# Kernel tuning notes

Hardware: AMD Instinct MI355X
Metric: run time of the kernel (lower is better)

## Reference

```python
import jax, jax.numpy as jnp
import numpy as np

N = 20000        # nodes
E = 640000       # edges (before self-loops)
F_IN = 128
HID = 64
HEADS = 4
F_OUT = 128
G = 64           # graphs in batch
NEG_SLOPE = 0.2  # PyG GATConv leaky_relu default


def setup_inputs() -> dict:
    key = jax.random.key(0)
    ks = jax.random.split(key, 16)
    s = 0.05
    x = jax.random.normal(ks[0], (N, F_IN), jnp.float32)
    edge_index = jax.random.randint(ks[1], (2, E), 0, N, dtype=jnp.int64)
    batch = jnp.sort(jax.random.randint(ks[2], (N,), 0, G, dtype=jnp.int64))
    # layer 1: F_IN -> HID x HEADS (concat)
    W1 = jax.random.normal(ks[3], (F_IN, HEADS * HID), jnp.float32) * s
    a_src1 = jax.random.normal(ks[4], (HEADS, HID), jnp.float32) * s
    a_dst1 = jax.random.normal(ks[5], (HEADS, HID), jnp.float32) * s
    b1 = jnp.zeros((HEADS * HID,), jnp.float32)
    # layer 2: HEADS*HID -> HID x HEADS (concat)
    W2 = jax.random.normal(ks[6], (HEADS * HID, HEADS * HID), jnp.float32) * s
    a_src2 = jax.random.normal(ks[7], (HEADS, HID), jnp.float32) * s
    a_dst2 = jax.random.normal(ks[8], (HEADS, HID), jnp.float32) * s
    b2 = jnp.zeros((HEADS * HID,), jnp.float32)
    # layer 3: HEADS*HID -> F_OUT, heads=1, concat=False (mean)
    W3 = jax.random.normal(ks[9], (HEADS * HID, F_OUT), jnp.float32) * s
    a_src3 = jax.random.normal(ks[10], (1, F_OUT), jnp.float32) * s
    a_dst3 = jax.random.normal(ks[11], (1, F_OUT), jnp.float32) * s
    b3 = jnp.zeros((F_OUT,), jnp.float32)
    return dict(x=x, edge_index=edge_index, batch=batch,
                W1=W1, a_src1=a_src1, a_dst1=a_dst1, b1=b1,
                W2=W2, a_src2=a_src2, a_dst2=a_dst2, b2=b2,
                W3=W3, a_src3=a_src3, a_dst3=a_dst3, b3=b3)


def _gat_layer(x, src, dst, W, a_s, a_d, b, heads, concat):
    n = x.shape[0]
    h = (x @ W).reshape(n, heads, -1)                # [N,H,C]
    alpha_s = (h * a_s[None]).sum(-1)                # [N,H]
    alpha_d = (h * a_d[None]).sum(-1)                # [N,H]
    e = jax.nn.leaky_relu(alpha_s[src] + alpha_d[dst], NEG_SLOPE)  # [E,H]
    # segment softmax over incoming edges of each dst node
    m = jax.ops.segment_max(e, dst, num_segments=n)
    ex = jnp.exp(e - m[dst])
    denom = jax.ops.segment_sum(ex, dst, num_segments=n)
    alpha = ex / (denom[dst] + 1e-16)                # [E,H]
    out = jax.ops.segment_sum(alpha[:, :, None] * h[src], dst, num_segments=n)  # [N,H,C]
    out = out.reshape(n, -1) if concat else out.mean(axis=1)
    return out + b


def reference(x, edge_index, batch, W1, a_src1, a_dst1, b1,
              W2, a_src2, a_dst2, b2, W3, a_src3, a_dst3, b3):
    n = x.shape[0]
    # add self loops (PyG GATConv default add_self_loops=True)
    loop = jnp.arange(n, dtype=edge_index.dtype)
    src = jnp.concatenate([edge_index[0], loop])
    dst = jnp.concatenate([edge_index[1], loop])

    h = _gat_layer(x, src, dst, W1, a_src1, a_dst1, b1, HEADS, True)
    h = jax.nn.elu(h)
    h = _gat_layer(h, src, dst, W2, a_src2, a_dst2, b2, HEADS, True)
    h = jax.nn.elu(h)
    h = _gat_layer(h, src, dst, W3, a_src3, a_dst3, b3, 1, False)

    # global mean pool over graphs
    sums = jax.ops.segment_sum(h, batch, num_segments=G)
    cnts = jax.ops.segment_sum(jnp.ones((n, 1), h.dtype), batch, num_segments=G)
    graph_embedding = sums / jnp.maximum(cnts, 1.0)
    return graph_embedding, h
```

## Files before the change

### kernel.cpp

```cpp
#include <hip/hip_runtime.h>
#include <hip/hip_bf16.h>
#include <math.h>

#define N_NODES 20000
#define N_EDGES 640000
#define ET_EDGES (N_EDGES + N_NODES)
#define G_GRAPHS 64
#define NEG_SLOPE 0.2f

typedef __attribute__((ext_vector_type(8))) short s8v;
typedef __attribute__((ext_vector_type(4))) float f4v;

__device__ __forceinline__ unsigned short bf_hi(float f) {
    union { float f; unsigned int u; } c; c.f = f;
    unsigned int r = (c.u + 0x7fffu + ((c.u >> 16) & 1u)) >> 16;
    return (unsigned short)r;
}
__device__ __forceinline__ float bf_f(unsigned short h) {
    union { unsigned int u; float f; } c; c.u = ((unsigned int)h) << 16;
    return c.f;
}


__global__ void hist_dst(const int* __restrict__ ei, int* __restrict__ cnt,
                         const int* __restrict__ batch, int* __restrict__ gstart) {
    int j = blockIdx.x * blockDim.x + threadIdx.x;
    if (blockIdx.x == 0 && threadIdx.x <= G_GRAPHS) {
        int g = threadIdx.x;
        int lo = 0, hi = N_NODES;
        while (lo < hi) {
            int mid = (lo + hi) >> 1;
            if (batch[mid] < g) lo = mid + 1; else hi = mid;
        }
        gstart[g] = lo;
    }
    if (j >= ET_EDGES) return;
    int d = (j < N_EDGES) ? ei[N_EDGES + j] : (j - N_EDGES);
    atomicAdd(&cnt[d], 1);
}

__global__ __launch_bounds__(1024) void scan_rowptr(const int* __restrict__ cnt,
                                                    int* __restrict__ row_ptr) {
    __shared__ int lds[N_NODES];
    __shared__ int sums[1024];
    const int n = N_NODES;
    const int CH = (n + 1023) / 1024;
    int t = threadIdx.x;
    for (int i = t; i < n; i += 1024) lds[i] = cnt[i];
    __syncthreads();
    int base = t * CH;
    int s = 0;
    for (int i = 0; i < CH; ++i) {
        int idx = base + i;
        if (idx < n) s += lds[idx];
    }
    sums[t] = s;
    __syncthreads();
    for (int o = 1; o < 1024; o <<= 1) {
        int v = (t >= o) ? sums[t - o] : 0;
        __syncthreads();
        sums[t] += v;
        __syncthreads();
    }
    int run = (t == 0) ? 0 : sums[t - 1];
    for (int i = 0; i < CH; ++i) {
        int idx = base + i;
        if (idx < n) { int c = lds[idx]; lds[idx] = run; run += c; }
    }
    __syncthreads();
    for (int i = t; i < n; i += 1024) row_ptr[i] = lds[i];
    if (t == 1023) row_ptr[n] = sums[1023];
}

__global__ void fill_csr(const int* __restrict__ ei, const int* __restrict__ row_ptr,
                         int* __restrict__ cur, int* __restrict__ col) {
    int j = blockIdx.x * blockDim.x + threadIdx.x;
    if (j >= ET_EDGES) return;
    int s, d;
    if (j < N_EDGES) { s = ei[j]; d = ei[N_EDGES + j]; }
    else             { s = d = j - N_EDGES; }
    int pos = row_ptr[d] + atomicAdd(&cur[d], 1);
    col[pos] = s;
}


__global__ void prep_split(const float* __restrict__ x,
                           const float* __restrict__ W1, const float* __restrict__ W2,
                           const float* __restrict__ W3,
                           unsigned short* __restrict__ xh, unsigned short* __restrict__ xl,
                           unsigned short* __restrict__ w1h, unsigned short* __restrict__ w1l,
                           unsigned short* __restrict__ w2h, unsigned short* __restrict__ w2l,
                           unsigned short* __restrict__ w3h, unsigned short* __restrict__ w3l,
                           int* __restrict__ cntcur, float* __restrict__ gout,
                           float* __restrict__ a3z) {
    int idx = blockIdx.x * blockDim.x + threadIdx.x;
    if (idx < 640000) {
        int i = idx * 4;
        float4 v = *(const float4*)&x[i];
        ushort4 h, l;
        h.x = bf_hi(v.x); l.x = bf_hi(v.x - bf_f(h.x));
        h.y = bf_hi(v.y); l.y = bf_hi(v.y - bf_f(h.y));
        h.z = bf_hi(v.z); l.z = bf_hi(v.z - bf_f(h.z));
        h.w = bf_hi(v.w); l.w = bf_hi(v.w - bf_f(h.w));
        *(ushort4*)&xh[i] = h;
        *(ushort4*)&xl[i] = l;
        return;
    }
    idx -= 640000;
    if (idx < 32768) {
        int k = idx / 256, n = idx % 256;
        float v = W1[idx];
        unsigned short h = bf_hi(v);
        w1h[n * 128 + k] = h;
        w1l[n * 128 + k] = bf_hi(v - bf_f(h));
        return;
    }
    idx -= 32768;
    if (idx < 65536) {
        int k = idx / 256, n = idx % 256;
        float v = W2[idx];
        unsigned short h = bf_hi(v);
        w2h[n * 256 + k] = h;
        w2l[n * 256 + k] = bf_hi(v - bf_f(h));
        return;
    }
    idx -= 65536;
    if (idx < 32768) {
        int k = idx / 128, n = idx % 128;
        float v = W3[idx];
        unsigned short h = bf_hi(v);
        w3h[n * 256 + k] = h;
        w3l[n * 256 + k] = bf_hi(v - bf_f(h));
        return;
    }
    idx -= 32768;
    if (idx < 10000) {
        *(int4*)&cntcur[idx * 4] = make_int4(0, 0, 0, 0);
        return;
    }
    idx -= 10000;
    if (idx < 2048) {
        *(float4*)&gout[idx * 4] = make_float4(0.f, 0.f, 0.f, 0.f);
        return;
    }
    idx -= 2048;
    if (idx < 10000) {
        *(float4*)&a3z[idx * 4] = make_float4(0.f, 0.f, 0.f, 0.f);
    }
}


#define LDT 40

template <int CPH>
__global__ __launch_bounds__(256) void gemm_split(
        const unsigned short* __restrict__ Ah, const unsigned short* __restrict__ Al,
        const unsigned short* __restrict__ Bh, const unsigned short* __restrict__ Bl,
        float* __restrict__ C, int M, int Nc, int K,
        const float* __restrict__ a_src, const float* __restrict__ a_dst,
        float* __restrict__ asT, float* __restrict__ adT) {
    __shared__ unsigned short lAh[128 * LDT];
    __shared__ unsigned short lAl[128 * LDT];
    __shared__ unsigned short lBh[128 * LDT];
    __shared__ unsigned short lBl[128 * LDT];
    int bm = blockIdx.x * 128, bn = blockIdx.y * 128;
    int t = threadIdx.x, w = t >> 6, lane = t & 63;
    int wm = (w >> 1) * 64, wn = (w & 1) * 64;

    f4v acc[4][4] = {};

    int sr = t >> 1, sk = (t & 1) << 4;
    int ar = bm + sr; if (ar >= M) ar = M - 1;
    const unsigned short* pAh = Ah + (size_t)ar * K + sk;
    const unsigned short* pAl = Al + (size_t)ar * K + sk;
    const unsigned short* pBh = Bh + (size_t)(bn + sr) * K + sk;
    const unsigned short* pBl = Bl + (size_t)(bn + sr) * K + sk;

    int fr = lane & 15, fk = (lane >> 4) << 3;

    uint4 vh0 = *(const uint4*)(pAh + 0);
    uint4 vh1 = *(const uint4*)(pAh + 8);
    uint4 vl0 = *(const uint4*)(pAl + 0);
    uint4 vl1 = *(const uint4*)(pAl + 8);
    uint4 wh0 = *(const uint4*)(pBh + 0);
    uint4 wh1 = *(const uint4*)(pBh + 8);
    uint4 wl0 = *(const uint4*)(pBl + 0);
    uint4 wl1 = *(const uint4*)(pBl + 8);

    for (int k0 = 0; k0 < K; k0 += 32) {
        __syncthreads();
        *(uint4*)&lAh[sr * LDT + sk]     = vh0;
        *(uint4*)&lAh[sr * LDT + sk + 8] = vh1;
        *(uint4*)&lAl[sr * LDT + sk]     = vl0;
        *(uint4*)&lAl[sr * LDT + sk + 8] = vl1;
        *(uint4*)&lBh[sr * LDT + sk]     = wh0;
        *(uint4*)&lBh[sr * LDT + sk + 8] = wh1;
        *(uint4*)&lBl[sr * LDT + sk]     = wl0;
        *(uint4*)&lBl[sr * LDT + sk + 8] = wl1;
        __syncthreads();

        int kn = k0 + 32;
        if (kn < K) {
            vh0 = *(const uint4*)(pAh + kn);
            vh1 = *(const uint4*)(pAh + kn + 8);
            vl0 = *(const uint4*)(pAl + kn);
            vl1 = *(const uint4*)(pAl + kn + 8);
            wh0 = *(const uint4*)(pBh + kn);
            wh1 = *(const uint4*)(pBh + kn + 8);
            wl0 = *(const uint4*)(pBl + kn);
            wl1 = *(const uint4*)(pBl + kn + 8);
        }

        s8v a_h[4], a_l[4], b_h[4], b_l[4];
        #pragma unroll
        for (int mi = 0; mi < 4; ++mi) {
            a_h[mi] = *(const s8v*)&lAh[(wm + mi * 16 + fr) * LDT + fk];
            a_l[mi] = *(const s8v*)&lAl[(wm + mi * 16 + fr) * LDT + fk];
        }
        #pragma unroll
        for (int nj = 0; nj < 4; ++nj) {
            b_h[nj] = *(const s8v*)&lBh[(wn + nj * 16 + fr) * LDT + fk];
            b_l[nj] = *(const s8v*)&lBl[(wn + nj * 16 + fr) * LDT + fk];
        }
        #pragma unroll
        for (int mi = 0; mi < 4; ++mi)
            #pragma unroll
            for (int nj = 0; nj < 4; ++nj) {
                acc[mi][nj] = __builtin_amdgcn_mfma_f32_16x16x32_bf16(
                    a_h[mi], b_h[nj], acc[mi][nj], 0, 0, 0);
                acc[mi][nj] = __builtin_amdgcn_mfma_f32_16x16x32_bf16(
                    a_h[mi], b_l[nj], acc[mi][nj], 0, 0, 0);
                acc[mi][nj] = __builtin_amdgcn_mfma_f32_16x16x32_bf16(
                    a_l[mi], b_h[nj], acc[mi][nj], 0, 0, 0);
            }
    }

    #pragma unroll
    for (int mi = 0; mi < 4; ++mi)
        #pragma unroll
        for (int nj = 0; nj < 4; ++nj) {
            int row0 = bm + wm + mi * 16 + (lane >> 4) * 4;
            int colc = bn + wn + nj * 16 + (lane & 15);
            #pragma unroll
            for (int q = 0; q < 4; ++q) {
                int r = row0 + q;
                if (r < M) C[(size_t)r * Nc + colc] = acc[mi][nj][q];
            }
        }

    float av_s[4], av_d[4];
    #pragma unroll
    for (int nj = 0; nj < 4; ++nj) {
        int aidx = bn + wn + nj * 16 + fr;
        av_s[nj] = a_src[aidx];
        av_d[nj] = a_dst[aidx];
    }
    int head = (bn + wn) / CPH;
    #pragma unroll
    for (int mi = 0; mi < 4; ++mi) {
        #pragma unroll
        for (int q = 0; q < 4; ++q) {
            float ps = acc[mi][0][q] * av_s[0] + acc[mi][1][q] * av_s[1]
                     + acc[mi][2][q] * av_s[2] + acc[mi][3][q] * av_s[3];
            float pd = acc[mi][0][q] * av_d[0] + acc[mi][1][q] * av_d[1]
                     + acc[mi][2][q] * av_d[2] + acc[mi][3][q] * av_d[3];
            #pragma unroll
            for (int o = 1; o < 16; o <<= 1) {
                ps += __shfl_xor(ps, o);
                pd += __shfl_xor(pd, o);
            }
            if (fr == 0) {
                int r = bm + wm + mi * 16 + (lane >> 4) * 4 + q;
                if (r < M) {
                    if (CPH == 64) {
                        asT[(size_t)head * M + r] = ps;
                        adT[(size_t)head * M + r] = pd;
                    } else {
                        atomicAdd(&asT[r], ps);
                        atomicAdd(&adT[r], pd);
                    }
                }
            }
        }
    }
}


template <int NSLICE, int SCH, int F, int HEADS, bool DO_ELU, bool SPLIT>
__global__ __launch_bounds__(256) void gat_aggregate_sliced(
        const float* __restrict__ h,
        const float* __restrict__ asT,
        const float* __restrict__ adT,
        const int* __restrict__ row_ptr,
        const int* __restrict__ col,
        const float* __restrict__ bias,
        float* __restrict__ out,
        unsigned short* __restrict__ oh,
        unsigned short* __restrict__ ol) {
    constexpr int CL = SCH / 4;
    constexpr int E  = 64 / CL;
    constexpr int CPH = F / HEADS;
    __shared__ int   s_off[4][64];
    __shared__ float s_p[4][64];
    int slice = blockIdx.x & (NSLICE - 1);
    int ng = blockIdx.x >> 2;
    int wid = threadIdx.x >> 6, lane = threadIdx.x & 63;
    int v = ng * 4 + wid;
    if (v >= N_NODES) return;
    int head = (slice * SCH) / CPH;
    int eg = lane / CL, cl = lane % CL;
    int r0 = row_ptr[v], r1 = row_ptr[v + 1];
    float ad = adT[head * N_NODES + v];
    const float* asrc = asT + head * N_NODES;
    float acc[4] = {};
    float lsum = 0.f;
    const char* hb = (const char*)(h + slice * SCH + cl * 4);

#define GATHER4(gg)                                                        \
    {                                                                      \
        int k0 = ((gg) + 0) * E + eg;                                      \
        int k1 = ((gg) + 1) * E + eg;                                      \
        int k2 = ((gg) + 2) * E + eg;                                      \
        int k3 = ((gg) + 3) * E + eg;                                      \
        float p0 = s_p[wid][k0]; int o0 = s_off[wid][k0];                  \
        float p1 = s_p[wid][k1]; int o1 = s_off[wid][k1];                  \
        float p2 = s_p[wid][k2]; int o2 = s_off[wid][k2];                  \
        float p3 = s_p[wid][k3]; int o3 = s_off[wid][k3];                  \
        float4 h0 = *(const float4*)(hb + o0);                             \
        float4 h1 = *(const float4*)(hb + o1);                             \
        float4 h2 = *(const float4*)(hb + o2);                             \
        float4 h3 = *(const float4*)(hb + o3);                             \
        acc[0] = fmaf(p0, h0.x, acc[0]);                                   \
        acc[1] = fmaf(p0, h0.y, acc[1]);                                   \
        acc[2] = fmaf(p0, h0.z, acc[2]);                                   \
        acc[3] = fmaf(p0, h0.w, acc[3]);                                   \
        acc[0] = fmaf(p1, h1.x, acc[0]);                                   \
        acc[1] = fmaf(p1, h1.y, acc[1]);                                   \
        acc[2] = fmaf(p1, h1.z, acc[2]);                                   \
        acc[3] = fmaf(p1, h1.w, acc[3]);                                   \
        acc[0] = fmaf(p2, h2.x, acc[0]);                                   \
        acc[1] = fmaf(p2, h2.y, acc[1]);                                   \
        acc[2] = fmaf(p2, h2.z, acc[2]);                                   \
        acc[3] = fmaf(p2, h2.w, acc[3]);                                   \
        acc[0] = fmaf(p3, h3.x, acc[0]);                                   \
        acc[1] = fmaf(p3, h3.y, acc[1]);                                   \
        acc[2] = fmaf(p3, h3.z, acc[2]);                                   \
        acc[3] = fmaf(p3, h3.w, acc[3]);                                   \
    }

    for (int base = r0; base < r1; base += 64) {
        int j = base + lane;
        bool valid = j < r1;
        int s = col[valid ? j : r0];
        float e = asrc[s] + ad;
        e = (e > 0.f) ? e : NEG_SLOPE * e;
        float p = valid ? __expf(e) : 0.f;
        lsum += p;
        s_p[wid][lane] = p;
        s_off[wid][lane] = s * (F * 4);

        int nk = min(64, r1 - base);
        int nkg = (nk + E - 1) / E;
        int g = 0;
        for (; g + 4 <= nkg; g += 4) GATHER4(g);
        if (g < nkg) GATHER4(g);
    }
#undef GATHER4

    #pragma unroll
    for (int o = 32; o; o >>= 1) lsum += __shfl_xor(lsum, o);
    #pragma unroll
    for (int c = 0; c < 4; ++c) {
        #pragma unroll
        for (int o = CL; o < 64; o <<= 1) acc[c] += __shfl_xor(acc[c], o);
    }
    if (eg == 0) {
        float inv = 1.f / (lsum + 1e-16f);
        int ch0 = slice * SCH + cl * 4;
        float o4[4];
        #pragma unroll
        for (int c = 0; c < 4; ++c) {
            float o = acc[c] * inv + bias[ch0 + c];
            if (DO_ELU) o = (o > 0.f) ? o : expm1f(o);
            o4[c] = o;
        }
        if constexpr (SPLIT) {
            ushort4 hv4, lv4;
            hv4.x = bf_hi(o4[0]); lv4.x = bf_hi(o4[0] - bf_f(hv4.x));
            hv4.y = bf_hi(o4[1]); lv4.y = bf_hi(o4[1] - bf_f(hv4.y));
            hv4.z = bf_hi(o4[2]); lv4.z = bf_hi(o4[2] - bf_f(hv4.z));
            hv4.w = bf_hi(o4[3]); lv4.w = bf_hi(o4[3] - bf_f(hv4.w));
            *(ushort4*)&oh[(size_t)v * F + ch0] = hv4;
            *(ushort4*)&ol[(size_t)v * F + ch0] = lv4;
        } else {
            *(float4*)&out[(size_t)v * F + ch0] =
                make_float4(o4[0], o4[1], o4[2], o4[3]);
        }
    }
}


__global__ void pool_mean4(const float* __restrict__ hout, const int* __restrict__ gstart,
                           float* __restrict__ gout) {
    int g = blockIdx.x;
    int q = blockIdx.y;
    int c = threadIdx.x;
    int off = gstart[g], end = gstart[g + 1];
    float inv = 1.f / fmaxf((float)(end - off), 1.0f);
    float s = 0.f;
    for (int i = off + q; i < end; i += 4) s += hout[(size_t)i * 128 + c];
    atomicAdd(&gout[g * 128 + c], s * inv);
}


static inline size_t align_up(size_t x, size_t a) { return (x + a - 1) & ~(a - 1); }

extern "C" void kernel_launch(void* const* d_in, const int* in_sizes, int n_in,
                              void* d_out, int out_size, void* d_ws, size_t ws_size,
                              hipStream_t stream) {
    const float* x   = (const float*)d_in[0];
    const int*   ei  = (const int*)d_in[1];
    const int*   bat = (const int*)d_in[2];
    const float* W1  = (const float*)d_in[3];
    const float* as1 = (const float*)d_in[4];
    const float* ad1 = (const float*)d_in[5];
    const float* b1  = (const float*)d_in[6];
    const float* W2  = (const float*)d_in[7];
    const float* as2 = (const float*)d_in[8];
    const float* ad2 = (const float*)d_in[9];
    const float* b2  = (const float*)d_in[10];
    const float* W3  = (const float*)d_in[11];
    const float* as3 = (const float*)d_in[12];
    const float* ad3 = (const float*)d_in[13];
    const float* b3  = (const float*)d_in[14];

    float* gout = (float*)d_out;
    float* hout = (float*)d_out + G_GRAPHS * 128;

    char* w = (char*)d_ws;
    size_t o = 0;
    float* bufA = (float*)(w + o);           o = align_up(o + (size_t)N_NODES * 256 * 4, 256);
    unsigned short* Bh = (unsigned short*)(w + o); o = align_up(o + (size_t)N_NODES * 256 * 2, 256);
    unsigned short* Bl = (unsigned short*)(w + o); o = align_up(o + (size_t)N_NODES * 256 * 2, 256);
    unsigned short* xh = (unsigned short*)(w + o); o = align_up(o + (size_t)N_NODES * 128 * 2, 256);
    unsigned short* xl = (unsigned short*)(w + o); o = align_up(o + (size_t)N_NODES * 128 * 2, 256);
    unsigned short* Wt1h = (unsigned short*)(w + o); o = align_up(o + (size_t)256 * 128 * 2, 256);
    unsigned short* Wt1l = (unsigned short*)(w + o); o = align_up(o + (size_t)256 * 128 * 2, 256);
    unsigned short* Wt2h = (unsigned short*)(w + o); o = align_up(o + (size_t)256 * 256 * 2, 256);
    unsigned short* Wt2l = (unsigned short*)(w + o); o = align_up(o + (size_t)256 * 256 * 2, 256);
    unsigned short* Wt3h = (unsigned short*)(w + o); o = align_up(o + (size_t)128 * 256 * 2, 256);
    unsigned short* Wt3l = (unsigned short*)(w + o); o = align_up(o + (size_t)128 * 256 * 2, 256);
    float* alpha = (float*)(w + o);
    float* asv1 = alpha;
    float* adv1 = alpha + 4 * N_NODES;
    float* asv2 = alpha + 8 * N_NODES;
    float* adv2 = alpha + 12 * N_NODES;
    float* asv3 = alpha + 16 * N_NODES;
    float* adv3 = alpha + 17 * N_NODES;
    o = align_up(o + (size_t)18 * N_NODES * 4, 256);
    int* row_ptr = (int*)(w + o);  o = align_up(o + (size_t)(N_NODES + 1) * 4, 256);
    int* col     = (int*)(w + o);  o = align_up(o + (size_t)ET_EDGES * 4, 256);
    int* cnt     = (int*)(w + o);  o += (size_t)N_NODES * 4;
    int* cur     = (int*)(w + o);  o = align_up(o + (size_t)N_NODES * 4, 256);
    int* gstart  = (int*)(w + o);  o = align_up(o + (size_t)(G_GRAPHS + 1) * 4, 256);

    {
        int total = 640000 + 32768 + 65536 + 32768 + 10000 + 2048 + 10000;
        prep_split<<<(total + 255) / 256, 256, 0, stream>>>(
            x, W1, W2, W3, xh, xl, Wt1h, Wt1l, Wt2h, Wt2l, Wt3h, Wt3l, cnt, gout, asv3);
    }
    hist_dst<<<(ET_EDGES + 255) / 256, 256, 0, stream>>>(ei, cnt, bat, gstart);
    scan_rowptr<<<1, 1024, 0, stream>>>(cnt, row_ptr);
    fill_csr<<<(ET_EDGES + 255) / 256, 256, 0, stream>>>(ei, row_ptr, cur, col);

    int gm = (N_NODES + 127) / 128;
    int nb = (N_NODES + 3) / 4;
    int nbs = nb * 4;

    gemm_split<64><<<dim3(gm, 2), 256, 0, stream>>>(
        xh, xl, Wt1h, Wt1l, bufA, N_NODES, 256, 128, as1, ad1, asv1, adv1);
    gat_aggregate_sliced<4, 64, 256, 4, true, true><<<nbs, 256, 0, stream>>>(
        bufA, asv1, adv1, row_ptr, col, b1, nullptr, Bh, Bl);

    gemm_split<64><<<dim3(gm, 2), 256, 0, stream>>>(
        Bh, Bl, Wt2h, Wt2l, bufA, N_NODES, 256, 256, as2, ad2, asv2, adv2);
    gat_aggregate_sliced<4, 64, 256, 4, true, true><<<nbs, 256, 0, stream>>>(
        bufA, asv2, adv2, row_ptr, col, b2, nullptr, Bh, Bl);

    gemm_split<128><<<dim3(gm, 1), 256, 0, stream>>>(
        Bh, Bl, Wt3h, Wt3l, bufA, N_NODES, 128, 256, as3, ad3, asv3, adv3);
    gat_aggregate_sliced<4, 32, 128, 1, false, false><<<nbs, 256, 0, stream>>>(
        bufA, asv3, adv3, row_ptr, col, b3, hout, nullptr, nullptr);

    pool_mean4<<<dim3(G_GRAPHS, 4), 128, 0, stream>>>(hout, gstart, gout);
}
```

Before: 399.1 us.

## Fuse CSR build and prep into one cooperative kernel with grid syncs

Replaces the four preprocessing launches (prep_split, hist_dst, scan_rowptr, fill_csr) with a single cooperative kernel of 1024 blocks that separates the phases with grid-wide syncs. The single-block scan over 20000 counts becomes a two-level scan: per-block partial sums, one block scanning the block totals, then each block writing its own row_ptr chunk. This is meant to cut launch gaps and the serial scan cost. In exchange it relies on cooperative launch co-residency for all 1024 blocks, adds five grid.sync barriers, and has one thread per block write its row_ptr chunk serially.

```diff
diff --git a/kernel.cpp b/kernel.cpp
--- a/kernel.cpp
+++ b/kernel.cpp
@@ -1,6 +1,9 @@
 #include <hip/hip_runtime.h>
 #include <hip/hip_bf16.h>
+#include <hip/hip_cooperative_groups.h>
 #include <math.h>
+
+namespace cg = cooperative_groups;
 
 #define N_NODES 20000
 #define N_EDGES 640000
@@ -8,6 +11,9 @@
 #define G_GRAPHS 64
 #define NEG_SLOPE 0.2f
 
+#define NBC 1024
+#define CHC ((N_NODES + NBC - 1) / NBC)
+
 typedef __attribute__((ext_vector_type(8))) short s8v;
 typedef __attribute__((ext_vector_type(4))) float f4v;
 
@@ -22,11 +28,89 @@
 }
 
 
-__global__ void hist_dst(const int* __restrict__ ei, int* __restrict__ cnt,
-                         const int* __restrict__ batch, int* __restrict__ gstart) {
-    int j = blockIdx.x * blockDim.x + threadIdx.x;
-    if (blockIdx.x == 0 && threadIdx.x <= G_GRAPHS) {
-        int g = threadIdx.x;
+__global__ void __launch_bounds__(256) build_all(
+        const float* __restrict__ x,
+        const float* __restrict__ W1, const float* __restrict__ W2,
+        const float* __restrict__ W3,
+        const int* __restrict__ ei, const int* __restrict__ batch,
+        unsigned short* __restrict__ xh, unsigned short* __restrict__ xl,
+        unsigned short* __restrict__ w1h, unsigned short* __restrict__ w1l,
+        unsigned short* __restrict__ w2h, unsigned short* __restrict__ w2l,
+        unsigned short* __restrict__ w3h, unsigned short* __restrict__ w3l,
+        int* __restrict__ cntcur,
+        float* __restrict__ gout, float* __restrict__ a3z,
+        int* __restrict__ row_ptr, int* __restrict__ col,
+        int* __restrict__ gstart, int* __restrict__ bsum) {
+    cg::grid_group grid = cg::this_grid();
+    __shared__ int l2[NBC];
+    __shared__ int ps[256];
+    int tid = blockIdx.x * blockDim.x + threadIdx.x;
+    int nth = gridDim.x * blockDim.x;
+    int* cnt = cntcur;
+    int* cur = cntcur + N_NODES;
+
+    for (int idx = tid; idx < 793120; idx += nth) {
+        int q = idx;
+        if (q < 640000) {
+            int i = q * 4;
+            float4 v = *(const float4*)&x[i];
+            ushort4 h, l;
+            h.x = bf_hi(v.x); l.x = bf_hi(v.x - bf_f(h.x));
+            h.y = bf_hi(v.y); l.y = bf_hi(v.y - bf_f(h.y));
+            h.z = bf_hi(v.z); l.z = bf_hi(v.z - bf_f(h.z));
+            h.w = bf_hi(v.w); l.w = bf_hi(v.w - bf_f(h.w));
+            *(ushort4*)&xh[i] = h;
+            *(ushort4*)&xl[i] = l;
+            continue;
+        }
+        q -= 640000;
+        if (q < 32768) {
+            int k = q / 256, n = q % 256;
+            float v = W1[q];
+            unsigned short h = bf_hi(v);
+            w1h[n * 128 + k] = h;
+            w1l[n * 128 + k] = bf_hi(v - bf_f(h));
+            continue;
+        }
+        q -= 32768;
+        if (q < 65536) {
+            int k = q / 256, n = q % 256;
+            float v = W2[q];
+            unsigned short h = bf_hi(v);
+            w2h[n * 256 + k] = h;
+            w2l[n * 256 + k] = bf_hi(v - bf_f(h));
+            continue;
+        }
+        q -= 65536;
+        if (q < 32768) {
+            int k = q / 128, n = q % 128;
+            float v = W3[q];
+            unsigned short h = bf_hi(v);
+            w3h[n * 256 + k] = h;
+            w3l[n * 256 + k] = bf_hi(v - bf_f(h));
+            continue;
+        }
+        q -= 32768;
+        if (q < 10000) {
+            *(int4*)&cntcur[q * 4] = make_int4(0, 0, 0, 0);
+            continue;
+        }
+        q -= 10000;
+        if (q < 2048) {
+            *(float4*)&gout[q * 4] = make_float4(0.f, 0.f, 0.f, 0.f);
+            continue;
+        }
+        q -= 2048;
+        *(float4*)&a3z[q * 4] = make_float4(0.f, 0.f, 0.f, 0.f);
+    }
+    grid.sync();
+
+    for (int j = tid; j < ET_EDGES; j += nth) {
+        int d = (j < N_EDGES) ? ei[N_EDGES + j] : (j - N_EDGES);
+        atomicAdd(&cnt[d], 1);
+    }
+    if (tid <= G_GRAPHS) {
+        int g = tid;
         int lo = 0, hi = N_NODES;
         while (lo < hi) {
             int mid = (lo + hi) >> 1;
@@ -34,118 +118,70 @@
         }
         gstart[g] = lo;
     }
-    if (j >= ET_EDGES) return;
-    int d = (j < N_EDGES) ? ei[N_EDGES + j] : (j - N_EDGES);
-    atomicAdd(&cnt[d], 1);
-}
-
-__global__ __launch_bounds__(1024) void scan_rowptr(const int* __restrict__ cnt,
-                                                    int* __restrict__ row_ptr) {
-    __shared__ int lds[N_NODES];
-    __shared__ int sums[1024];
-    const int n = N_NODES;
-    const int CH = (n + 1023) / 1024;
-    int t = threadIdx.x;
-    for (int i = t; i < n; i += 1024) lds[i] = cnt[i];
-    __syncthreads();
-    int base = t * CH;
-    int s = 0;
-    for (int i = 0; i < CH; ++i) {
-        int idx = base + i;
-        if (idx < n) s += lds[idx];
-    }
-    sums[t] = s;
-    __syncthreads();
-    for (int o = 1; o < 1024; o <<= 1) {
-        int v = (t >= o) ? sums[t - o] : 0;
+    grid.sync();
+
+    {
+        int t = threadIdx.x, b = blockIdx.x;
+        int s = 0;
+        int base = b * CHC;
+        for (int i = t; i < CHC; i += 256) {
+            int idx = base + i;
+            if (idx < N_NODES) s += cnt[idx];
+        }
+        ps[t] = s;
         __syncthreads();
-        sums[t] += v;
+        for (int o = 128; o; o >>= 1) {
+            if (t < o) ps[t] += ps[t + o];
+            __syncthreads();
+        }
+        if (t == 0) bsum[b] = ps[0];
+    }
+    grid.sync();
+
+    if (blockIdx.x == 0) {
+        int t = threadIdx.x;
+        for (int i = t; i < NBC; i += 256) l2[i] = bsum[i];
         __syncthreads();
-    }
-    int run = (t == 0) ? 0 : sums[t - 1];
-    for (int i = 0; i < CH; ++i) {
-        int idx = base + i;
-        if (idx < n) { int c = lds[idx]; lds[idx] = run; run += c; }
-    }
-    __syncthreads();
-    for (int i = t; i < n; i += 1024) row_ptr[i] = lds[i];
-    if (t == 1023) row_ptr[n] = sums[1023];
-}
-
-__global__ void fill_csr(const int* __restrict__ ei, const int* __restrict__ row_ptr,
-                         int* __restrict__ cur, int* __restrict__ col) {
-    int j = blockIdx.x * blockDim.x + threadIdx.x;
-    if (j >= ET_EDGES) return;
-    int s, d;
-    if (j < N_EDGES) { s = ei[j]; d = ei[N_EDGES + j]; }
-    else             { s = d = j - N_EDGES; }
-    int pos = row_ptr[d] + atomicAdd(&cur[d], 1);
-    col[pos] = s;
-}
-
-
-__global__ void prep_split(const float* __restrict__ x,
-                           const float* __restrict__ W1, const float* __restrict__ W2,
-                           const float* __restrict__ W3,
-                           unsigned short* __restrict__ xh, unsigned short* __restrict__ xl,
-                           unsigned short* __restrict__ w1h, unsigned short* __restrict__ w1l,
-                           unsigned short* __restrict__ w2h, unsigned short* __restrict__ w2l,
-                           unsigned short* __restrict__ w3h, unsigned short* __restrict__ w3l,
-                           int* __restrict__ cntcur, float* __restrict__ gout,
-                           float* __restrict__ a3z) {
-    int idx = blockIdx.x * blockDim.x + threadIdx.x;
-    if (idx < 640000) {
-        int i = idx * 4;
-        float4 v = *(const float4*)&x[i];
-        ushort4 h, l;
-        h.x = bf_hi(v.x); l.x = bf_hi(v.x - bf_f(h.x));
-        h.y = bf_hi(v.y); l.y = bf_hi(v.y - bf_f(h.y));
-        h.z = bf_hi(v.z); l.z = bf_hi(v.z - bf_f(h.z));
-        h.w = bf_hi(v.w); l.w = bf_hi(v.w - bf_f(h.w));
-        *(ushort4*)&xh[i] = h;
-        *(ushort4*)&xl[i] = l;
-        return;
-    }
-    idx -= 640000;
-    if (idx < 32768) {
-        int k = idx / 256, n = idx % 256;
-        float v = W1[idx];
-        unsigned short h = bf_hi(v);
-        w1h[n * 128 + k] = h;
-        w1l[n * 128 + k] = bf_hi(v - bf_f(h));
-        return;
-    }
-    idx -= 32768;
-    if (idx < 65536) {
-        int k = idx / 256, n = idx % 256;
-        float v = W2[idx];
-        unsigned short h = bf_hi(v);
-        w2h[n * 256 + k] = h;
-        w2l[n * 256 + k] = bf_hi(v - bf_f(h));
-        return;
-    }
-    idx -= 65536;
-    if (idx < 32768) {
-        int k = idx / 128, n = idx % 128;
-        float v = W3[idx];
-        unsigned short h = bf_hi(v);
-        w3h[n * 256 + k] = h;
-        w3l[n * 256 + k] = bf_hi(v - bf_f(h));
-        return;
-    }
-    idx -= 32768;
-    if (idx < 10000) {
-        *(int4*)&cntcur[idx * 4] = make_int4(0, 0, 0, 0);
-        return;
-    }
-    idx -= 10000;
-    if (idx < 2048) {
-        *(float4*)&gout[idx * 4] = make_float4(0.f, 0.f, 0.f, 0.f);
-        return;
-    }
-    idx -= 2048;
-    if (idx < 10000) {
-        *(float4*)&a3z[idx * 4] = make_float4(0.f, 0.f, 0.f, 0.f);
+        int s = 0;
+        #pragma unroll
+        for (int k = 0; k < NBC / 256; ++k) s += l2[t * (NBC / 256) + k];
+        ps[t] = s;
+        __syncthreads();
+        for (int o = 1; o < 256; o <<= 1) {
+            int v = (t >= o) ? ps[t - o] : 0;
+            __syncthreads();
+            ps[t] += v;
+            __syncthreads();
+        }
+        int run = (t == 0) ? 0 : ps[t - 1];
+        #pragma unroll
+        for (int k = 0; k < NBC / 256; ++k) {
+            int i = t * (NBC / 256) + k;
+            int c = l2[i]; l2[i] = run; run += c;
+        }
+        __syncthreads();
+        for (int i = t; i < NBC; i += 256) bsum[i] = l2[i];
+    }
+    grid.sync();
+
+    if (threadIdx.x == 0) {
+        int b = blockIdx.x;
+        int run = bsum[b];
+        int base = b * CHC;
+        for (int i = 0; i < CHC; ++i) {
+            int idx = base + i;
+            if (idx < N_NODES) { row_ptr[idx] = run; run += cnt[idx]; }
+        }
+        if (b == NBC - 1) row_ptr[N_NODES] = run;
+    }
+    grid.sync();
+
+    for (int j = tid; j < ET_EDGES; j += nth) {
+        int s, d;
+        if (j < N_EDGES) { s = ei[j]; d = ei[N_EDGES + j]; }
+        else             { s = d = j - N_EDGES; }
+        int pos = row_ptr[d] + atomicAdd(&cur[d], 1);
+        col[pos] = s;
     }
 }
 
@@ -463,15 +499,21 @@
     int* cnt     = (int*)(w + o);  o += (size_t)N_NODES * 4;
     int* cur     = (int*)(w + o);  o = align_up(o + (size_t)N_NODES * 4, 256);
     int* gstart  = (int*)(w + o);  o = align_up(o + (size_t)(G_GRAPHS + 1) * 4, 256);
+    int* bsum    = (int*)(w + o);  o = align_up(o + (size_t)NBC * 4, 256);
 
     {
-        int total = 640000 + 32768 + 65536 + 32768 + 10000 + 2048 + 10000;
-        prep_split<<<(total + 255) / 256, 256, 0, stream>>>(
-            x, W1, W2, W3, xh, xl, Wt1h, Wt1l, Wt2h, Wt2l, Wt3h, Wt3l, cnt, gout, asv3);
-    }
-    hist_dst<<<(ET_EDGES + 255) / 256, 256, 0, stream>>>(ei, cnt, bat, gstart);
-    scan_rowptr<<<1, 1024, 0, stream>>>(cnt, row_ptr);
-    fill_csr<<<(ET_EDGES + 255) / 256, 256, 0, stream>>>(ei, row_ptr, cur, col);
+        void* args[] = {
+            (void*)&x, (void*)&W1, (void*)&W2, (void*)&W3,
+            (void*)&ei, (void*)&bat,
+            (void*)&xh, (void*)&xl,
+            (void*)&Wt1h, (void*)&Wt1l, (void*)&Wt2h, (void*)&Wt2l,
+            (void*)&Wt3h, (void*)&Wt3l,
+            (void*)&cnt, (void*)&gout, (void*)&asv3,
+            (void*)&row_ptr, (void*)&col, (void*)&gstart, (void*)&bsum,
+        };
+        hipLaunchCooperativeKernel((const void*)build_all, dim3(NBC), dim3(256),
+                                   args, 0, stream);
+    }
 
     int gm = (N_NODES + 127) / 128;
     int nb = (N_NODES + 3) / 4;
```

Result: slower. 941.2 us (+135.9%).
